# Optimization experiments

Measured on AMD Instinct MI355X. Metric: run time of the kernel, lower is better.

The kernel has to match this reference:

```python
import jax, jax.numpy as jnp
import numpy as np

N = 50000
E = 300000
D_IN = 128
H = 256
D_OUT = 256


def _glorot(key, shape):
    fan_in, fan_out = shape[0], shape[1]
    lim = float(np.sqrt(6.0 / (fan_in + fan_out)))
    return jax.random.uniform(key, shape, jnp.float32, -lim, lim)


def setup_inputs() -> dict:
    key = jax.random.key(0)
    ks = jax.random.split(key, 12)
    x = jax.random.normal(ks[0], (N, D_IN), jnp.float32)
    edge_index = jax.random.randint(ks[1], (2, E), 0, N, jnp.int64)
    return {
        "x": x,
        "edge_index": edge_index,
        "W1": _glorot(ks[2], (D_IN, H)),  "b1": jnp.zeros((H,), jnp.float32),
        "Wg1": _glorot(ks[3], (H, H)),    "bg1": jnp.zeros((H,), jnp.float32),
        "Wg2": _glorot(ks[4], (H, H)),    "bg2": jnp.zeros((H,), jnp.float32),
        "W2": _glorot(ks[5], (H, H)),     "b2": jnp.zeros((H,), jnp.float32),
        "W3": _glorot(ks[6], (H, D_OUT)), "b3": jnp.zeros((D_OUT,), jnp.float32),
    }


def _gcn_conv(h, src, dst, W, b):
    # PyG GCNConv: h' = D^-1/2 (A + I) D^-1/2 (h W) + b, deg counted at target with self-loops
    h = h @ W                                           # [N, H]
    deg = jnp.zeros((N,), h.dtype).at[dst].add(1.0) + 1.0
    dinv = jax.lax.rsqrt(deg)                           # deg^-1/2, [N]
    norm = dinv[src] * dinv[dst]                        # [E]
    msg = h[src] * norm[:, None]                        # gather + scale, [E, H]
    agg = jax.ops.segment_sum(msg, dst, num_segments=N)  # scatter-add
    agg = agg + h * (dinv * dinv)[:, None]              # self-loop contribution (norm = 1/deg)
    return agg + b


def reference(x, edge_index, W1, b1, Wg1, bg1, Wg2, bg2, W2, b2, W3, b3):
    src, dst = edge_index[0], edge_index[1]
    h = jax.nn.relu(x @ W1 + b1)
    h = jax.nn.relu(_gcn_conv(h, src, dst, Wg1, bg1))
    h = jax.nn.relu(_gcn_conv(h, src, dst, Wg2, bg2))
    h = jax.nn.relu(h @ W2 + b2)
    return jax.nn.softmax(h @ W3 + b3, axis=1)
```

## Files before the change

### kernel.cpp

```cpp
#include <hip/hip_runtime.h>
#include <math.h>

#define HDIM 256

typedef float floatx4 __attribute__((ext_vector_type(4)));
typedef __bf16 bf16x8 __attribute__((ext_vector_type(8)));
typedef unsigned short ushortx4 __attribute__((ext_vector_type(4)));
typedef unsigned short ushortx8 __attribute__((ext_vector_type(8)));

#define AS1C(p) ((const __attribute__((address_space(1))) void*)(p))
#define AS3(p)  ((__attribute__((address_space(3))) void*)(p))

__device__ inline unsigned short bf16_rn(float f) {
  unsigned u = __float_as_uint(f);
  return (unsigned short)((u + 0x7FFFu + ((u >> 16) & 1u)) >> 16);
}

__device__ inline void split_f32(float f, unsigned short& h, unsigned short& l) {
  unsigned short hb = bf16_rn(f);
  float hf = __uint_as_float(((unsigned)hb) << 16);
  h = hb;
  l = bf16_rn(f - hf);
}

// ... 92 lines not shown
void scan_final_kernel(const int* __restrict__ deg, const int* __restrict__ boff,
                       int* __restrict__ rowptr, int* __restrict__ cursor, int n) {
  __shared__ int sm[256];
  int t = threadIdx.x;
  int idx = blockIdx.x * 256 + t;
  int v = (idx < n) ? deg[idx] : 0;
  sm[t] = v;
  __syncthreads();
  for (int off = 1; off < 256; off <<= 1) {
    int a = (t >= off) ? sm[t - off] : 0;
    __syncthreads();
    sm[t] += a;
    __syncthreads();
  }
  int excl = sm[t] - v + boff[blockIdx.x];
  if (idx < n) { rowptr[idx] = excl; cursor[idx] = excl; }
}

__global__ __launch_bounds__(256)
void fill_csr_kernel(const int* __restrict__ ei, const float* __restrict__ dinv,
                     int* __restrict__ cursor, int* __restrict__ col,
                     float* __restrict__ wsrc, int E) {
  int e = blockIdx.x * 256 + threadIdx.x;
  if (e < E) {
    int s = ei[e];
    int d = ei[E + e];
    int p = atomicAdd(&cursor[d], 1);
    col[p] = s;
    wsrc[p] = dinv[s];
  }
}


template<bool BIAS, bool RELU>
__global__ __launch_bounds__(512, 4)
void mfma_gemm_sA(const float* __restrict__ A,
                  const unsigned short* __restrict__ SWH, const unsigned short* __restrict__ SWL,
                  const float* __restrict__ bias,
                  unsigned short* __restrict__ CH, unsigned short* __restrict__ CL,
                  int M, int K) {
  __shared__ __align__(16) unsigned short AsH[4096];
  __shared__ __align__(16) unsigned short AsL[4096];
  __shared__ __align__(16) unsigned short BsH[8192];
  __shared__ __align__(16) unsigned short BsL[8192];

  const int tid = threadIdx.x;
  const int w = tid >> 6;
  const int l = tid & 63;
  const int l15 = l & 15;
  const int quad = l >> 4;
  const int wm = w & 1;
  const int wn = w >> 1;
  const int bm = blockIdx.x * 128;
  const int ktc = K >> 5;
  const int chunksPerCb = ktc * 512;

  floatx4 acc[4][4];
#pragma unroll
  for (int i = 0; i < 4; ++i)
#pragma unroll
    for (int j = 0; j < 4; ++j) acc[i][j] = (floatx4){0.f, 0.f, 0.f, 0.f};

  const int arow = tid >> 2;
  const int ap = tid & 3;
  const int akc = ap ^ (arow & 3) ^ ((arow >> 2) & 3);
  int agrow = bm + arow;
  if (agrow > M - 1) agrow = M - 1;
  const float* agp = A + (size_t)agrow * K + akc * 8;

  for (int kt = 0; kt < ktc; ++kt) {
    float4 f0 = *(const float4*)(agp + kt * 32);
    float4 f1 = *(const float4*)(agp + kt * 32 + 4);

    __syncthreads();

#pragma unroll
    for (int j = 0; j < 2; ++j) {
      int pos = j * 512 + w * 64 + l;
      int kc = pos >> 8;
      int within = pos & 255;
      int cb = within >> 7;
      int colL = within & 127;
      size_t gi = (size_t)cb * chunksPerCb + (size_t)kt * 512 + kc * 128 + colL;
      __builtin_amdgcn_global_load_lds(AS1C(SWH + gi * 8),
                                       AS3(&BsH[(j * 512 + w * 64) * 8]), 16, 0, 0);
      __builtin_amdgcn_global_load_lds(AS1C(SWL + gi * 8),
                                       AS3(&BsL[(j * 512 + w * 64) * 8]), 16, 0, 0);
    }

    {
      float f[8] = {f0.x, f0.y, f0.z, f0.w, f1.x, f1.y, f1.z, f1.w};
      ushortx8 hh, ll;
#pragma unroll
      for (int e = 0; e < 8; ++e) {
        unsigned short h, lo;
        split_f32(f[e], h, lo);
        hh[e] = h;
        ll[e] = lo;
      }
      *(ushortx8*)&AsH[(size_t)tid * 8] = hh;
      *(ushortx8*)&AsL[(size_t)tid * 8] = ll;
    }

    __syncthreads();

    bf16x8 aH[4], aL[4];
#pragma unroll
    for (int fi = 0; fi < 4; ++fi) {
      int r = wm * 64 + fi * 16 + l15;
      int sw = quad ^ (r & 3) ^ ((r >> 2) & 3);
      aH[fi] = *(const bf16x8*)&AsH[(r * 4 + sw) * 8];
      aL[fi] = *(const bf16x8*)&AsL[(r * 4 + sw) * 8];
    }
#pragma unroll
    for (int fj = 0; fj < 4; ++fj) {
      int colG = wn * 64 + fj * 16 + l15;
      int cidx = quad * 256 + colG;
      bf16x8 bh = *(const bf16x8*)&BsH[cidx * 8];
      bf16x8 bl = *(const bf16x8*)&BsL[cidx * 8];
#pragma unroll
      for (int fi = 0; fi < 4; ++fi) {
        floatx4 t = acc[fi][fj];
        t = __builtin_amdgcn_mfma_f32_16x16x32_bf16(aH[fi], bl, t, 0, 0, 0);
        t = __builtin_amdgcn_mfma_f32_16x16x32_bf16(aL[fi], bh, t, 0, 0, 0);
        t = __builtin_amdgcn_mfma_f32_16x16x32_bf16(aH[fi], bh, t, 0, 0, 0);
        acc[fi][fj] = t;
      }
    }
  }

  float bcol[4];
#pragma unroll
  for (int fj = 0; fj < 4; ++fj)
    bcol[fj] = BIAS ? bias[wn * 64 + fj * 16 + l15] : 0.f;

#pragma unroll
  for (int fi = 0; fi < 4; ++fi) {
    int rb = bm + wm * 64 + fi * 16 + quad * 4;
#pragma unroll
    for (int r = 0; r < 4; ++r) {
      int row = rb + r;
      if (row < M) {
        size_t base = (size_t)row * HDIM + wn * 64 + l15;
#pragma unroll
        for (int fj = 0; fj < 4; ++fj) {
          float v = acc[fi][fj][r] + bcol[fj];
          if (RELU) v = fmaxf(v, 0.f);
          unsigned short h, lo;
          split_f32(v, h, lo);
          CH[base + fj * 16] = h;
          CL[base + fj * 16] = lo;
        }
      }
    }
  }
}


template<bool BIAS, bool RELU, bool SPLIT_OUT>
__global__ __launch_bounds__(512, 4)
void mfma_gemm_p(const unsigned short* __restrict__ AH, const unsigned short* __restrict__ AL,
                 const unsigned short* __restrict__ SWH, const unsigned short* __restrict__ SWL,
                 const float* __restrict__ bias,
                 float* __restrict__ C, unsigned short* __restrict__ CH,
                 unsigned short* __restrict__ CL, int M, int K) {
  __shared__ __align__(16) unsigned short AsH[4096];
  __shared__ __align__(16) unsigned short AsL[4096];
  __shared__ __align__(16) unsigned short BsH[8192];
  __shared__ __align__(16) unsigned short BsL[8192];

  const int tid = threadIdx.x;
  const int w = tid >> 6;
  const int l = tid & 63;
  const int l15 = l & 15;
  const int quad = l >> 4;
  const int wm = w & 1;
  const int wn = w >> 1;
  const int bm = blockIdx.x * 128;
  const int ktc = K >> 5;
  const int chunksPerCb = ktc * 512;

  floatx4 acc[4][4];
#pragma unroll
  for (int i = 0; i < 4; ++i)
#pragma unroll
    for (int j = 0; j < 4; ++j) acc[i][j] = (floatx4){0.f, 0.f, 0.f, 0.f};

  for (int kt = 0; kt < ktc; ++kt) {
    __syncthreads();

    {
      int L = tid;
      int row = L >> 2;
      int p = L & 3;
      int kc = p ^ (row & 3) ^ ((row >> 2) & 3);
      int grow = bm + row;
      if (grow > M - 1) grow = M - 1;
      const unsigned short* gH = AH + (size_t)grow * K + kt * 32 + kc * 8;
      const unsigned short* gL = AL + (size_t)grow * K + kt * 32 + kc * 8;
      __builtin_amdgcn_global_load_lds(AS1C(gH), AS3(&AsH[(w * 64) * 8]), 16, 0, 0);
      __builtin_amdgcn_global_load_lds(AS1C(gL), AS3(&AsL[(w * 64) * 8]), 16, 0, 0);
    }
#pragma unroll
    for (int j = 0; j < 2; ++j) {
      int pos = j * 512 + w * 64 + l;
      int kc = pos >> 8;
      int within = pos & 255;
      int cb = within >> 7;
      int colL = within & 127;
      size_t gi = (size_t)cb * chunksPerCb + (size_t)kt * 512 + kc * 128 + colL;
      __builtin_amdgcn_global_load_lds(AS1C(SWH + gi * 8),
                                       AS3(&BsH[(j * 512 + w * 64) * 8]), 16, 0, 0);
      __builtin_amdgcn_global_load_lds(AS1C(SWL + gi * 8),
                                       AS3(&BsL[(j * 512 + w * 64) * 8]), 16, 0, 0);
    }

    __syncthreads();

    bf16x8 aH[4], aL[4];
#pragma unroll
    for (int fi = 0; fi < 4; ++fi) {
      int r = wm * 64 + fi * 16 + l15;
      int sw = quad ^ (r & 3) ^ ((r >> 2) & 3);
      aH[fi] = *(const bf16x8*)&AsH[(r * 4 + sw) * 8];
      aL[fi] = *(const bf16x8*)&AsL[(r * 4 + sw) * 8];
    }
#pragma unroll
    for (int fj = 0; fj < 4; ++fj) {
      int colG = wn * 64 + fj * 16 + l15;
      int cidx = quad * 256 + colG;
      bf16x8 bh = *(const bf16x8*)&BsH[cidx * 8];
      bf16x8 bl = *(const bf16x8*)&BsL[cidx * 8];
#pragma unroll
      for (int fi = 0; fi < 4; ++fi) {
        floatx4 t = acc[fi][fj];
        t = __builtin_amdgcn_mfma_f32_16x16x32_bf16(aH[fi], bl, t, 0, 0, 0);
        t = __builtin_amdgcn_mfma_f32_16x16x32_bf16(aL[fi], bh, t, 0, 0, 0);
        t = __builtin_amdgcn_mfma_f32_16x16x32_bf16(aH[fi], bh, t, 0, 0, 0);
        acc[fi][fj] = t;
      }
    }
  }

  float bcol[4];
#pragma unroll
  for (int fj = 0; fj < 4; ++fj)
    bcol[fj] = BIAS ? bias[wn * 64 + fj * 16 + l15] : 0.f;

#pragma unroll
  for (int fi = 0; fi < 4; ++fi) {
    int rb = bm + wm * 64 + fi * 16 + quad * 4;
#pragma unroll
    for (int r = 0; r < 4; ++r) {
      int row = rb + r;
      if (row < M) {
        size_t base = (size_t)row * HDIM + wn * 64 + l15;
        if (SPLIT_OUT) {
#pragma unroll
          for (int fj = 0; fj < 4; ++fj) {
            float v = acc[fi][fj][r] + bcol[fj];
            if (RELU) v = fmaxf(v, 0.f);
            unsigned short h, lo;
            split_f32(v, h, lo);
            CH[base + fj * 16] = h;
            CL[base + fj * 16] = lo;
          }
        } else {
#pragma unroll
          for (int fj = 0; fj < 4; ++fj) {
            float v = acc[fi][fj][r] + bcol[fj];
            if (RELU) v = fmaxf(v, 0.f);
            C[base + fj * 16] = v;
          }
        }
      }
    }
  }
}


__global__ __launch_bounds__(512, 4)
void mfma_gemm_softmax(const unsigned short* __restrict__ AH, const unsigned short* __restrict__ AL,
                       const unsigned short* __restrict__ SWH, const unsigned short* __restrict__ SWL,
                       const float* __restrict__ bias, float* __restrict__ out, int M, int K) {
  __shared__ __align__(16) unsigned short AsH[4096];
  __shared__ __align__(16) unsigned short AsL[4096];
  __shared__ __align__(16) unsigned short BsH[8192];
  __shared__ __align__(16) unsigned short BsL[8192];
  __shared__ float smax[128 * 4];
  __shared__ float ssum[128 * 4];

  const int tid = threadIdx.x;
  const int w = tid >> 6;
  const int l = tid & 63;
  const int l15 = l & 15;
  const int quad = l >> 4;
  const int wm = w & 1;
  const int wn = w >> 1;
  const int bm = blockIdx.x * 128;
  const int ktc = K >> 5;
  const int chunksPerCb = ktc * 512;

  floatx4 acc[4][4];
#pragma unroll
  for (int i = 0; i < 4; ++i)
#pragma unroll
    for (int j = 0; j < 4; ++j) acc[i][j] = (floatx4){0.f, 0.f, 0.f, 0.f};

  for (int kt = 0; kt < ktc; ++kt) {
    __syncthreads();

    {
      int L = tid;
      int row = L >> 2;
      int p = L & 3;
      int kc = p ^ (row & 3) ^ ((row >> 2) & 3);
      int grow = bm + row;
      if (grow > M - 1) grow = M - 1;
      const unsigned short* gH = AH + (size_t)grow * K + kt * 32 + kc * 8;
      const unsigned short* gL = AL + (size_t)grow * K + kt * 32 + kc * 8;
      __builtin_amdgcn_global_load_lds(AS1C(gH), AS3(&AsH[(w * 64) * 8]), 16, 0, 0);
      __builtin_amdgcn_global_load_lds(AS1C(gL), AS3(&AsL[(w * 64) * 8]), 16, 0, 0);
    }
#pragma unroll
    for (int j = 0; j < 2; ++j) {
      int pos = j * 512 + w * 64 + l;
      int kc = pos >> 8;
      int within = pos & 255;
      int cb = within >> 7;
      int colL = within & 127;
      size_t gi = (size_t)cb * chunksPerCb + (size_t)kt * 512 + kc * 128 + colL;
      __builtin_amdgcn_global_load_lds(AS1C(SWH + gi * 8),
                                       AS3(&BsH[(j * 512 + w * 64) * 8]), 16, 0, 0);
      __builtin_amdgcn_global_load_lds(AS1C(SWL + gi * 8),
                                       AS3(&BsL[(j * 512 + w * 64) * 8]), 16, 0, 0);
    }

    __syncthreads();

    bf16x8 aH[4], aL[4];
#pragma unroll
    for (int fi = 0; fi < 4; ++fi) {
      int r = wm * 64 + fi * 16 + l15;
      int sw = quad ^ (r & 3) ^ ((r >> 2) & 3);
      aH[fi] = *(const bf16x8*)&AsH[(r * 4 + sw) * 8];
      aL[fi] = *(const bf16x8*)&AsL[(r * 4 + sw) * 8];
    }
#pragma unroll
    for (int fj = 0; fj < 4; ++fj) {
      int colG = wn * 64 + fj * 16 + l15;
      int cidx = quad * 256 + colG;
      bf16x8 bh = *(const bf16x8*)&BsH[cidx * 8];
      bf16x8 bl = *(const bf16x8*)&BsL[cidx * 8];
#pragma unroll
      for (int fi = 0; fi < 4; ++fi) {
        floatx4 t = acc[fi][fj];
        t = __builtin_amdgcn_mfma_f32_16x16x32_bf16(aH[fi], bl, t, 0, 0, 0);
        t = __builtin_amdgcn_mfma_f32_16x16x32_bf16(aL[fi], bh, t, 0, 0, 0);
        t = __builtin_amdgcn_mfma_f32_16x16x32_bf16(aH[fi], bh, t, 0, 0, 0);
        acc[fi][fj] = t;
      }
    }
  }

  float bcol[4];
#pragma unroll
  for (int fj = 0; fj < 4; ++fj)
    bcol[fj] = bias[wn * 64 + fj * 16 + l15];

#pragma unroll
  for (int fi = 0; fi < 4; ++fi) {
#pragma unroll
    for (int r = 0; r < 4; ++r) {
      float mv = -3.4e38f;
#pragma unroll
      for (int fj = 0; fj < 4; ++fj) mv = fmaxf(mv, acc[fi][fj][r] + bcol[fj]);
#pragma unroll
      for (int off = 1; off < 16; off <<= 1) mv = fmaxf(mv, __shfl_xor(mv, off));
      int row = wm * 64 + fi * 16 + quad * 4 + r;
      if (l15 == 0) smax[row * 4 + wn] = mv;
    }
  }
  __syncthreads();

#pragma unroll
  for (int fi = 0; fi < 4; ++fi) {
#pragma unroll
    for (int r = 0; r < 4; ++r) {
      int row = wm * 64 + fi * 16 + quad * 4 + r;
      float gm = fmaxf(fmaxf(smax[row * 4 + 0], smax[row * 4 + 1]),
                       fmaxf(smax[row * 4 + 2], smax[row * 4 + 3]));
      float s = 0.f;
#pragma unroll
      for (int fj = 0; fj < 4; ++fj) {
        float p = expf(acc[fi][fj][r] + bcol[fj] - gm);
        acc[fi][fj][r] = p;
        s += p;
      }
#pragma unroll
      for (int off = 1; off < 16; off <<= 1) s += __shfl_xor(s, off);
      if (l15 == 0) ssum[row * 4 + wn] = s;
    }
  }
  __syncthreads();

#pragma unroll
  for (int fi = 0; fi < 4; ++fi) {
#pragma unroll
    for (int r = 0; r < 4; ++r) {
      int row = wm * 64 + fi * 16 + quad * 4 + r;
      int grow = bm + row;
      if (grow < M) {
        float inv = 1.0f / (ssum[row * 4 + 0] + ssum[row * 4 + 1] +
                            ssum[row * 4 + 2] + ssum[row * 4 + 3]);
        float* Cp = out + (size_t)grow * HDIM + wn * 64 + l15;
#pragma unroll
        for (int fj = 0; fj < 4; ++fj) Cp[fj * 16] = acc[fi][fj][r] * inv;
      }
    }
  }
}


__global__ __launch_bounds__(256)
void aggregate_b(const float* __restrict__ t, const float* __restrict__ dinv,
                 const int* __restrict__ rowptr, const int* __restrict__ col,
                 const float* __restrict__ wsrc, const float* __restrict__ bias,
                 unsigned short* __restrict__ OH, unsigned short* __restrict__ OL, int n) {
  int gw = (int)((blockIdx.x * 256 + threadIdx.x) >> 6);
  int lane = threadIdx.x & 63;
  if (gw >= n) return;
  float di = dinv[gw];
  float4 v = ((const float4*)(t + (size_t)gw * HDIM))[lane];
  float ss = di * di;
  float a0 = v.x * ss, a1 = v.y * ss, a2 = v.z * ss, a3 = v.w * ss;
  int e0 = rowptr[gw], e1 = rowptr[gw + 1];

  for (int base = e0; base < e1; base += 8) {
    int cs[8];
    float wv[8];
#pragma unroll
    for (int i = 0; i < 8; ++i) {
      int e = base + i;
      if (e > e1 - 1) e = e1 - 1;
      cs[i] = col[e];
      wv[i] = wsrc[e];
    }
    float wg[8];
#pragma unroll
    for (int i = 0; i < 8; ++i)
      wg[i] = (base + i < e1) ? wv[i] * di : 0.f;
    float4 rw[8];
#pragma unroll
    for (int i = 0; i < 8; ++i)
      rw[i] = ((const float4*)(t + (size_t)cs[i] * HDIM))[lane];
#pragma unroll
    for (int i = 0; i < 8; ++i) {
      a0 = fmaf(rw[i].x, wg[i], a0);
      a1 = fmaf(rw[i].y, wg[i], a1);
      a2 = fmaf(rw[i].z, wg[i], a2);
      a3 = fmaf(rw[i].w, wg[i], a3);
    }
  }

// ... 46 lines not shown
  int*   rowptr = (int*)alloc((size_t)(N + 1) * sizeof(int));
  int*   cursor = (int*)alloc((size_t)N * sizeof(int));
  int*   col    = (int*)alloc((size_t)E * sizeof(int));
  float* wcsr   = (float*)alloc((size_t)E * sizeof(float));
  const int nb  = (N + 255) / 256;
  int*   bsum   = (int*)alloc((size_t)nb * sizeof(int));
  int*   boff   = (int*)alloc((size_t)nb * sizeof(int));
  unsigned short* W1sH  = (unsigned short*)alloc((size_t)HDIM * K1 * 2);
  unsigned short* W1sL  = (unsigned short*)alloc((size_t)HDIM * K1 * 2);
  unsigned short* Wg1sH = (unsigned short*)alloc((size_t)HDIM * HDIM * 2);
  unsigned short* Wg1sL = (unsigned short*)alloc((size_t)HDIM * HDIM * 2);
  unsigned short* Wg2sH = (unsigned short*)alloc((size_t)HDIM * HDIM * 2);
  unsigned short* Wg2sL = (unsigned short*)alloc((size_t)HDIM * HDIM * 2);
  unsigned short* W2sH  = (unsigned short*)alloc((size_t)HDIM * HDIM * 2);
  unsigned short* W2sL  = (unsigned short*)alloc((size_t)HDIM * HDIM * 2);
  unsigned short* W3sH  = (unsigned short*)alloc((size_t)HDIM * HDIM * 2);
  unsigned short* W3sL  = (unsigned short*)alloc((size_t)HDIM * HDIM * 2);

  const int ge = (E + 255) / 256;

  const int prepChunks = K1 * 32 + 4 * HDIM * 32;
  prep_w_all<<<(prepChunks + 255) / 256, 256, 0, stream>>>(
      W1, W1sH, W1sL, K1, Wg1, Wg1sH, Wg1sL, Wg2, Wg2sH, Wg2sL,
      W2, W2sH, W2sL, W3, W3sH, W3sL);

  hipMemsetAsync(deg, 0, (size_t)N * sizeof(int), stream);
  deg_count_kernel<<<ge, 256, 0, stream>>>(ei, deg, E);
  block_sum_kernel<<<nb, 256, 0, stream>>>(deg, bsum, dinv, N);
  scan_bsums_kernel<<<1, 256, 0, stream>>>(bsum, boff, rowptr, nb, N);
  scan_final_kernel<<<nb, 256, 0, stream>>>(deg, boff, rowptr, cursor, N);
  fill_csr_kernel<<<ge, 256, 0, stream>>>(ei, dinv, cursor, col, wcsr, E);

  const int g128 = (N + 127) / 128;
  const int gagg = (N + 3) / 4;

  mfma_gemm_sA<true, true><<<g128, 512, 0, stream>>>(x, W1sH, W1sL, b1, PH, PL, N, K1);
  mfma_gemm_p<false, false, false><<<g128, 512, 0, stream>>>(PH, PL, Wg1sH, Wg1sL, nullptr, out, nullptr, nullptr, N, HDIM);
  aggregate_b<<<gagg, 256, 0, stream>>>(out, dinv, rowptr, col, wcsr, bg1, PH, PL, N);
  mfma_gemm_p<false, false, false><<<g128, 512, 0, stream>>>(PH, PL, Wg2sH, Wg2sL, nullptr, out, nullptr, nullptr, N, HDIM);
  aggregate_b<<<gagg, 256, 0, stream>>>(out, dinv, rowptr, col, wcsr, bg2, PH, PL, N);
  mfma_gemm_p<true, true, true><<<g128, 512, 0, stream>>>(PH, PL, W2sH, W2sL, b2, nullptr, PH, PL, N, HDIM);
  mfma_gemm_softmax<<<g128, 512, 0, stream>>>(PH, PL, W3sH, W3sL, b3, out, N, HDIM);
}
```

Before: 383.9 us.

## Double-buffer LDS tiles in the MFMA GEMM kernels to overlap loads with compute

The A and B shared-memory tiles in the three split-bf16 MFMA GEMM kernels are now double-buffered. The loads for the next K-tile are issued before the MFMAs on the current tile run, which removes one barrier per iteration and aims to hide global-to-LDS latency. The cost is twice the LDS per block, roughly 96KB, and the launch-bounds minimum is lowered from 4 to 2 blocks. That likely leaves only one resident 512-thread block per CU, so the kernels lose latency hiding across blocks.

```diff
diff --git a/kernel.cpp b/kernel.cpp
--- a/kernel.cpp
+++ b/kernel.cpp
@@ -149,16 +149,16 @@
 
 
 template<bool BIAS, bool RELU>
-__global__ __launch_bounds__(512, 4)
+__global__ __launch_bounds__(512, 2)
 void mfma_gemm_sA(const float* __restrict__ A,
                   const unsigned short* __restrict__ SWH, const unsigned short* __restrict__ SWL,
                   const float* __restrict__ bias,
                   unsigned short* __restrict__ CH, unsigned short* __restrict__ CL,
                   int M, int K) {
-  __shared__ __align__(16) unsigned short AsH[4096];
-  __shared__ __align__(16) unsigned short AsL[4096];
-  __shared__ __align__(16) unsigned short BsH[8192];
-  __shared__ __align__(16) unsigned short BsL[8192];
+  __shared__ __align__(16) unsigned short AsH[2][4096];
+  __shared__ __align__(16) unsigned short AsL[2][4096];
+  __shared__ __align__(16) unsigned short BsH[2][8192];
+  __shared__ __align__(16) unsigned short BsL[2][8192];
 
   const int tid = threadIdx.x;
   const int w = tid >> 6;
@@ -184,12 +184,7 @@
   if (agrow > M - 1) agrow = M - 1;
   const float* agp = A + (size_t)agrow * K + akc * 8;
 
-  for (int kt = 0; kt < ktc; ++kt) {
-    float4 f0 = *(const float4*)(agp + kt * 32);
-    float4 f1 = *(const float4*)(agp + kt * 32 + 4);
-
-    __syncthreads();
-
+  auto stageB = [&](int kt, int buf) {
 #pragma unroll
     for (int j = 0; j < 2; ++j) {
       int pos = j * 512 + w * 64 + l;
@@ -199,41 +194,58 @@
       int colL = within & 127;
       size_t gi = (size_t)cb * chunksPerCb + (size_t)kt * 512 + kc * 128 + colL;
       __builtin_amdgcn_global_load_lds(AS1C(SWH + gi * 8),
-                                       AS3(&BsH[(j * 512 + w * 64) * 8]), 16, 0, 0);
+                                       AS3(&BsH[buf][(j * 512 + w * 64) * 8]), 16, 0, 0);
       __builtin_amdgcn_global_load_lds(AS1C(SWL + gi * 8),
-                                       AS3(&BsL[(j * 512 + w * 64) * 8]), 16, 0, 0);
-    }
-
-    {
-      float f[8] = {f0.x, f0.y, f0.z, f0.w, f1.x, f1.y, f1.z, f1.w};
-      ushortx8 hh, ll;
-#pragma unroll
-      for (int e = 0; e < 8; ++e) {
-        unsigned short h, lo;
-        split_f32(f[e], h, lo);
-        hh[e] = h;
-        ll[e] = lo;
-      }
-      *(ushortx8*)&AsH[(size_t)tid * 8] = hh;
-      *(ushortx8*)&AsL[(size_t)tid * 8] = ll;
-    }
-
-    __syncthreads();
+                                       AS3(&BsL[buf][(j * 512 + w * 64) * 8]), 16, 0, 0);
+    }
+  };
+
+  auto writeA = [&](float4 f0, float4 f1, int buf) {
+    float f[8] = {f0.x, f0.y, f0.z, f0.w, f1.x, f1.y, f1.z, f1.w};
+    ushortx8 hh, ll;
+#pragma unroll
+    for (int e = 0; e < 8; ++e) {
+      unsigned short h, lo;
+      split_f32(f[e], h, lo);
+      hh[e] = h;
+      ll[e] = lo;
+    }
+    *(ushortx8*)&AsH[buf][(size_t)tid * 8] = hh;
+    *(ushortx8*)&AsL[buf][(size_t)tid * 8] = ll;
+  };
+
+  {
+    float4 f0 = *(const float4*)(agp);
+    float4 f1 = *(const float4*)(agp + 4);
+    stageB(0, 0);
+    writeA(f0, f1, 0);
+  }
+  __syncthreads();
+  int cur = 0;
+
+#pragma unroll 1
+  for (int kt = 0; kt < ktc; ++kt) {
+    if (kt + 1 < ktc) {
+      float4 f0 = *(const float4*)(agp + (kt + 1) * 32);
+      float4 f1 = *(const float4*)(agp + (kt + 1) * 32 + 4);
+      stageB(kt + 1, cur ^ 1);
+      writeA(f0, f1, cur ^ 1);
+    }
 
     bf16x8 aH[4], aL[4];
 #pragma unroll
     for (int fi = 0; fi < 4; ++fi) {
       int r = wm * 64 + fi * 16 + l15;
       int sw = quad ^ (r & 3) ^ ((r >> 2) & 3);
-      aH[fi] = *(const bf16x8*)&AsH[(r * 4 + sw) * 8];
-      aL[fi] = *(const bf16x8*)&AsL[(r * 4 + sw) * 8];
+      aH[fi] = *(const bf16x8*)&AsH[cur][(r * 4 + sw) * 8];
+      aL[fi] = *(const bf16x8*)&AsL[cur][(r * 4 + sw) * 8];
     }
 #pragma unroll
     for (int fj = 0; fj < 4; ++fj) {
       int colG = wn * 64 + fj * 16 + l15;
       int cidx = quad * 256 + colG;
-      bf16x8 bh = *(const bf16x8*)&BsH[cidx * 8];
-      bf16x8 bl = *(const bf16x8*)&BsL[cidx * 8];
+      bf16x8 bh = *(const bf16x8*)&BsH[cur][cidx * 8];
+      bf16x8 bl = *(const bf16x8*)&BsL[cur][cidx * 8];
 #pragma unroll
       for (int fi = 0; fi < 4; ++fi) {
         floatx4 t = acc[fi][fj];
@@ -243,6 +255,9 @@
         acc[fi][fj] = t;
       }
     }
+
+    __syncthreads();
+    cur ^= 1;
   }
 
   float bcol[4];
@@ -274,16 +289,16 @@
 
 
 template<bool BIAS, bool RELU, bool SPLIT_OUT>
-__global__ __launch_bounds__(512, 4)
+__global__ __launch_bounds__(512, 2)
 void mfma_gemm_p(const unsigned short* __restrict__ AH, const unsigned short* __restrict__ AL,
                  const unsigned short* __restrict__ SWH, const unsigned short* __restrict__ SWL,
                  const float* __restrict__ bias,
                  float* __restrict__ C, unsigned short* __restrict__ CH,
                  unsigned short* __restrict__ CL, int M, int K) {
-  __shared__ __align__(16) unsigned short AsH[4096];
-  __shared__ __align__(16) unsigned short AsL[4096];
-  __shared__ __align__(16) unsigned short BsH[8192];
-  __shared__ __align__(16) unsigned short BsL[8192];
+  __shared__ __align__(16) unsigned short AsH[2][4096];
+  __shared__ __align__(16) unsigned short AsL[2][4096];
+  __shared__ __align__(16) unsigned short BsH[2][8192];
+  __shared__ __align__(16) unsigned short BsL[2][8192];
 
   const int tid = threadIdx.x;
   const int w = tid >> 6;
@@ -302,20 +317,17 @@
 #pragma unroll
     for (int j = 0; j < 4; ++j) acc[i][j] = (floatx4){0.f, 0.f, 0.f, 0.f};
 
-  for (int kt = 0; kt < ktc; ++kt) {
-    __syncthreads();
-
+  auto stage = [&](int kt, int buf) {
     {
-      int L = tid;
-      int row = L >> 2;
-      int p = L & 3;
+      int row = tid >> 2;
+      int p = tid & 3;
       int kc = p ^ (row & 3) ^ ((row >> 2) & 3);
       int grow = bm + row;
       if (grow > M - 1) grow = M - 1;
       const unsigned short* gH = AH + (size_t)grow * K + kt * 32 + kc * 8;
       const unsigned short* gL = AL + (size_t)grow * K + kt * 32 + kc * 8;
-      __builtin_amdgcn_global_load_lds(AS1C(gH), AS3(&AsH[(w * 64) * 8]), 16, 0, 0);
-      __builtin_amdgcn_global_load_lds(AS1C(gL), AS3(&AsL[(w * 64) * 8]), 16, 0, 0);
+      __builtin_amdgcn_global_load_lds(AS1C(gH), AS3(&AsH[buf][(w * 64) * 8]), 16, 0, 0);
+      __builtin_amdgcn_global_load_lds(AS1C(gL), AS3(&AsL[buf][(w * 64) * 8]), 16, 0, 0);
     }
 #pragma unroll
     for (int j = 0; j < 2; ++j) {
@@ -326,27 +338,34 @@
       int colL = within & 127;
       size_t gi = (size_t)cb * chunksPerCb + (size_t)kt * 512 + kc * 128 + colL;
       __builtin_amdgcn_global_load_lds(AS1C(SWH + gi * 8),
-                                       AS3(&BsH[(j * 512 + w * 64) * 8]), 16, 0, 0);
+                                       AS3(&BsH[buf][(j * 512 + w * 64) * 8]), 16, 0, 0);
       __builtin_amdgcn_global_load_lds(AS1C(SWL + gi * 8),
-                                       AS3(&BsL[(j * 512 + w * 64) * 8]), 16, 0, 0);
-    }
-
-    __syncthreads();
+                                       AS3(&BsL[buf][(j * 512 + w * 64) * 8]), 16, 0, 0);
+    }
+  };
+
+  stage(0, 0);
+  __syncthreads();
+  int cur = 0;
+
+#pragma unroll 1
+  for (int kt = 0; kt < ktc; ++kt) {
+    if (kt + 1 < ktc) stage(kt + 1, cur ^ 1);
 
     bf16x8 aH[4], aL[4];
 #pragma unroll
     for (int fi = 0; fi < 4; ++fi) {
       int r = wm * 64 + fi * 16 + l15;
       int sw = quad ^ (r & 3) ^ ((r >> 2) & 3);
-      aH[fi] = *(const bf16x8*)&AsH[(r * 4 + sw) * 8];
-      aL[fi] = *(const bf16x8*)&AsL[(r * 4 + sw) * 8];
+      aH[fi] = *(const bf16x8*)&AsH[cur][(r * 4 + sw) * 8];
+      aL[fi] = *(const bf16x8*)&AsL[cur][(r * 4 + sw) * 8];
     }
 #pragma unroll
     for (int fj = 0; fj < 4; ++fj) {
       int colG = wn * 64 + fj * 16 + l15;
       int cidx = quad * 256 + colG;
-      bf16x8 bh = *(const bf16x8*)&BsH[cidx * 8];
-      bf16x8 bl = *(const bf16x8*)&BsL[cidx * 8];
+      bf16x8 bh = *(const bf16x8*)&BsH[cur][cidx * 8];
+      bf16x8 bl = *(const bf16x8*)&BsL[cur][cidx * 8];
 #pragma unroll
       for (int fi = 0; fi < 4; ++fi) {
         floatx4 t = acc[fi][fj];
@@ -356,6 +375,9 @@
         acc[fi][fj] = t;
       }
     }
+
+    __syncthreads();
+    cur ^= 1;
   }
 
   float bcol[4];
@@ -395,14 +417,14 @@
 }
 
 
-__global__ __launch_bounds__(512, 4)
+__global__ __launch_bounds__(512, 2)
 void mfma_gemm_softmax(const unsigned short* __restrict__ AH, const unsigned short* __restrict__ AL,
                        const unsigned short* __restrict__ SWH, const unsigned short* __restrict__ SWL,
                        const float* __restrict__ bias, float* __restrict__ out, int M, int K) {
-  __shared__ __align__(16) unsigned short AsH[4096];
-  __shared__ __align__(16) unsigned short AsL[4096];
-  __shared__ __align__(16) unsigned short BsH[8192];
-  __shared__ __align__(16) unsigned short BsL[8192];
+  __shared__ __align__(16) unsigned short AsH[2][4096];
+  __shared__ __align__(16) unsigned short AsL[2][4096];
+  __shared__ __align__(16) unsigned short BsH[2][8192];
+  __shared__ __align__(16) unsigned short BsL[2][8192];
   __shared__ float smax[128 * 4];
   __shared__ float ssum[128 * 4];
 
@@ -423,20 +445,17 @@
 #pragma unroll
     for (int j = 0; j < 4; ++j) acc[i][j] = (floatx4){0.f, 0.f, 0.f, 0.f};
 
-  for (int kt = 0; kt < ktc; ++kt) {
-    __syncthreads();
-
+  auto stage = [&](int kt, int buf) {
     {
-      int L = tid;
-      int row = L >> 2;
-      int p = L & 3;
+      int row = tid >> 2;
+      int p = tid & 3;
       int kc = p ^ (row & 3) ^ ((row >> 2) & 3);
       int grow = bm + row;
       if (grow > M - 1) grow = M - 1;
       const unsigned short* gH = AH + (size_t)grow * K + kt * 32 + kc * 8;
       const unsigned short* gL = AL + (size_t)grow * K + kt * 32 + kc * 8;
-      __builtin_amdgcn_global_load_lds(AS1C(gH), AS3(&AsH[(w * 64) * 8]), 16, 0, 0);
-      __builtin_amdgcn_global_load_lds(AS1C(gL), AS3(&AsL[(w * 64) * 8]), 16, 0, 0);
+      __builtin_amdgcn_global_load_lds(AS1C(gH), AS3(&AsH[buf][(w * 64) * 8]), 16, 0, 0);
+      __builtin_amdgcn_global_load_lds(AS1C(gL), AS3(&AsL[buf][(w * 64) * 8]), 16, 0, 0);
     }
 #pragma unroll
     for (int j = 0; j < 2; ++j) {
@@ -447,27 +466,34 @@
       int colL = within & 127;
       size_t gi = (size_t)cb * chunksPerCb + (size_t)kt * 512 + kc * 128 + colL;
       __builtin_amdgcn_global_load_lds(AS1C(SWH + gi * 8),
-                                       AS3(&BsH[(j * 512 + w * 64) * 8]), 16, 0, 0);
+                                       AS3(&BsH[buf][(j * 512 + w * 64) * 8]), 16, 0, 0);
       __builtin_amdgcn_global_load_lds(AS1C(SWL + gi * 8),
-                                       AS3(&BsL[(j * 512 + w * 64) * 8]), 16, 0, 0);
-    }
-
-    __syncthreads();
+                                       AS3(&BsL[buf][(j * 512 + w * 64) * 8]), 16, 0, 0);
+    }
+  };
+
+  stage(0, 0);
+  __syncthreads();
+  int cur = 0;
+
+#pragma unroll 1
+  for (int kt = 0; kt < ktc; ++kt) {
+    if (kt + 1 < ktc) stage(kt + 1, cur ^ 1);
 
     bf16x8 aH[4], aL[4];
 #pragma unroll
     for (int fi = 0; fi < 4; ++fi) {
       int r = wm * 64 + fi * 16 + l15;
       int sw = quad ^ (r & 3) ^ ((r >> 2) & 3);
-      aH[fi] = *(const bf16x8*)&AsH[(r * 4 + sw) * 8];
-      aL[fi] = *(const bf16x8*)&AsL[(r * 4 + sw) * 8];
+      aH[fi] = *(const bf16x8*)&AsH[cur][(r * 4 + sw) * 8];
+      aL[fi] = *(const bf16x8*)&AsL[cur][(r * 4 + sw) * 8];
     }
 #pragma unroll
     for (int fj = 0; fj < 4; ++fj) {
       int colG = wn * 64 + fj * 16 + l15;
       int cidx = quad * 256 + colG;
-      bf16x8 bh = *(const bf16x8*)&BsH[cidx * 8];
-      bf16x8 bl = *(const bf16x8*)&BsL[cidx * 8];
+      bf16x8 bh = *(const bf16x8*)&BsH[cur][cidx * 8];
+      bf16x8 bl = *(const bf16x8*)&BsL[cur][cidx * 8];
 #pragma unroll
       for (int fi = 0; fi < 4; ++fi) {
         floatx4 t = acc[fi][fj];
@@ -477,6 +503,9 @@
         acc[fi][fj] = t;
       }
     }
+
+    __syncthreads();
+    cur ^= 1;
   }
 
   float bcol[4];
```

After: 426.3 us. 11.0% more time.

## Fuse back-to-back dense GEMMs and keep the intermediate tile in LDS

Applied to the files above, without the earlier changes.

Adds a two-stage fused GEMM kernel that computes the first product, applies bias and ReLU, and feeds the result straight into the second GEMM through shared memory. It is used for x@W1 followed by @Wg1, and for @W2 followed by @W3 with softmax. This removes the global write and re-read of two full N×256 split-bf16 intermediates and two kernel launches. In exchange the fused kernel holds two accumulator sets, so launch bounds drop to 2 blocks per CU, and only one wave column writes each A tile per k-step while the others wait. The aggregation launches are also split into two half-range launches, which adds launch overhead without an obvious benefit.

```diff
diff --git a/kernel.cpp b/kernel.cpp
--- a/kernel.cpp
+++ b/kernel.cpp
@@ -148,13 +148,283 @@
 }
 
 
-template<bool BIAS, bool RELU>
+template<bool P1F32, bool SOFTMX>
+__global__ __launch_bounds__(512, 2)
+void fused_gemm2(const float* __restrict__ A32,
+                 const unsigned short* __restrict__ APH, const unsigned short* __restrict__ APL,
+                 const unsigned short* __restrict__ SW1H, const unsigned short* __restrict__ SW1L,
+                 const float* __restrict__ bias1,
+                 const unsigned short* __restrict__ SW2H, const unsigned short* __restrict__ SW2L,
+                 const float* __restrict__ bias2,
+                 float* __restrict__ outC, int M, int K1) {
+  __shared__ __align__(16) unsigned short AsH[4096];
+  __shared__ __align__(16) unsigned short AsL[4096];
+  __shared__ __align__(16) unsigned short BsH[8192];
+  __shared__ __align__(16) unsigned short BsL[8192];
+  __shared__ float smax[128 * 4];
+  __shared__ float ssum[128 * 4];
+
+  const int tid = threadIdx.x;
+  const int w = tid >> 6;
+  const int l = tid & 63;
+  const int l15 = l & 15;
+  const int quad = l >> 4;
+  const int wm = w & 1;
+  const int wn = w >> 1;
+  const int bm = blockIdx.x * 128;
+  const int ktc1 = K1 >> 5;
+  const int cPc1 = ktc1 * 512;
+
+  floatx4 acc1[4][4];
+#pragma unroll
+  for (int i = 0; i < 4; ++i)
+#pragma unroll
+    for (int j = 0; j < 4; ++j) acc1[i][j] = (floatx4){0.f, 0.f, 0.f, 0.f};
+
+  const int arow = tid >> 2;
+  const int ap = tid & 3;
+  const int akc = ap ^ (arow & 3) ^ ((arow >> 2) & 3);
+  int agrow = bm + arow;
+  if (agrow > M - 1) agrow = M - 1;
+  const float* agp = P1F32 ? (A32 + (size_t)agrow * K1 + akc * 8) : nullptr;
+
+  for (int kt = 0; kt < ktc1; ++kt) {
+    float4 f0, f1;
+    if (P1F32) {
+      f0 = *(const float4*)(agp + kt * 32);
+      f1 = *(const float4*)(agp + kt * 32 + 4);
+    }
+
+    __syncthreads();
+
+#pragma unroll
+    for (int j = 0; j < 2; ++j) {
+      int pos = j * 512 + w * 64 + l;
+      int kc = pos >> 8;
+      int within = pos & 255;
+      int cb = within >> 7;
+      int colL = within & 127;
+      size_t gi = (size_t)cb * cPc1 + (size_t)kt * 512 + kc * 128 + colL;
+      __builtin_amdgcn_global_load_lds(AS1C(SW1H + gi * 8),
+                                       AS3(&BsH[(j * 512 + w * 64) * 8]), 16, 0, 0);
+      __builtin_amdgcn_global_load_lds(AS1C(SW1L + gi * 8),
+                                       AS3(&BsL[(j * 512 + w * 64) * 8]), 16, 0, 0);
+    }
+
+    if (P1F32) {
+      float f[8] = {f0.x, f0.y, f0.z, f0.w, f1.x, f1.y, f1.z, f1.w};
+      ushortx8 hh, ll;
+#pragma unroll
+      for (int e = 0; e < 8; ++e) {
+        unsigned short h, lo;
+        split_f32(f[e], h, lo);
+        hh[e] = h;
+        ll[e] = lo;
+      }
+      *(ushortx8*)&AsH[(size_t)tid * 8] = hh;
+      *(ushortx8*)&AsL[(size_t)tid * 8] = ll;
+    } else {
+      int row = tid >> 2;
+      int p = tid & 3;
+      int kc = p ^ (row & 3) ^ ((row >> 2) & 3);
+      int grow = bm + row;
+      if (grow > M - 1) grow = M - 1;
+      const unsigned short* gH = APH + (size_t)grow * K1 + kt * 32 + kc * 8;
+      const unsigned short* gL = APL + (size_t)grow * K1 + kt * 32 + kc * 8;
+      __builtin_amdgcn_global_load_lds(AS1C(gH), AS3(&AsH[(w * 64) * 8]), 16, 0, 0);
+      __builtin_amdgcn_global_load_lds(AS1C(gL), AS3(&AsL[(w * 64) * 8]), 16, 0, 0);
+    }
+
+    __syncthreads();
+
+    bf16x8 aH[4], aL[4];
+#pragma unroll
+    for (int fi = 0; fi < 4; ++fi) {
+      int r = wm * 64 + fi * 16 + l15;
+      int sw = quad ^ (r & 3) ^ ((r >> 2) & 3);
+      aH[fi] = *(const bf16x8*)&AsH[(r * 4 + sw) * 8];
+      aL[fi] = *(const bf16x8*)&AsL[(r * 4 + sw) * 8];
+    }
+#pragma unroll
+    for (int fj = 0; fj < 4; ++fj) {
+      int colG = wn * 64 + fj * 16 + l15;
+      int cidx = quad * 256 + colG;
+      bf16x8 bh = *(const bf16x8*)&BsH[cidx * 8];
+      bf16x8 bl = *(const bf16x8*)&BsL[cidx * 8];
+#pragma unroll
+      for (int fi = 0; fi < 4; ++fi) {
+        floatx4 t = acc1[fi][fj];
+        t = __builtin_amdgcn_mfma_f32_16x16x32_bf16(aH[fi], bl, t, 0, 0, 0);
+        t = __builtin_amdgcn_mfma_f32_16x16x32_bf16(aL[fi], bh, t, 0, 0, 0);
+        t = __builtin_amdgcn_mfma_f32_16x16x32_bf16(aH[fi], bh, t, 0, 0, 0);
+        acc1[fi][fj] = t;
+      }
+    }
+  }
+
+  float bcol1[4];
+#pragma unroll
+  for (int fj = 0; fj < 4; ++fj)
+    bcol1[fj] = bias1[wn * 64 + fj * 16 + l15];
+
+  floatx4 acc2[4][4];
+#pragma unroll
+  for (int i = 0; i < 4; ++i)
+#pragma unroll
+    for (int j = 0; j < 4; ++j) acc2[i][j] = (floatx4){0.f, 0.f, 0.f, 0.f};
+
+  const int cPc2 = 8 * 512;
+
+  for (int kt2 = 0; kt2 < 8; ++kt2) {
+    __syncthreads();
+
+    if (wn == (kt2 >> 1)) {
+      int fjb = (kt2 & 1) * 2;
+#pragma unroll
+      for (int fjo = 0; fjo < 2; ++fjo) {
+        int fj = fjb + fjo;
+        int cl = fjo * 16 + l15;
+        int kc = cl >> 3;
+        int e = cl & 7;
+#pragma unroll
+        for (int fi = 0; fi < 4; ++fi) {
+#pragma unroll
+          for (int r = 0; r < 4; ++r) {
+            int R = wm * 64 + fi * 16 + quad * 4 + r;
+            int p = kc ^ (R & 3) ^ ((R >> 2) & 3);
+            float v = fmaxf(acc1[fi][fj][r] + bcol1[fj], 0.f);
+            unsigned short h, lo;
+            split_f32(v, h, lo);
+            AsH[(R * 4 + p) * 8 + e] = h;
+            AsL[(R * 4 + p) * 8 + e] = lo;
+          }
+        }
+      }
+    }
+
+#pragma unroll
+    for (int j = 0; j < 2; ++j) {
+      int pos = j * 512 + w * 64 + l;
+      int kc = pos >> 8;
+      int within = pos & 255;
+      int cb = within >> 7;
+      int colL = within & 127;
+      size_t gi = (size_t)cb * cPc2 + (size_t)kt2 * 512 + kc * 128 + colL;
+      __builtin_amdgcn_global_load_lds(AS1C(SW2H + gi * 8),
+                                       AS3(&BsH[(j * 512 + w * 64) * 8]), 16, 0, 0);
+      __builtin_amdgcn_global_load_lds(AS1C(SW2L + gi * 8),
+                                       AS3(&BsL[(j * 512 + w * 64) * 8]), 16, 0, 0);
+    }
+
+    __syncthreads();
+
+    bf16x8 aH[4], aL[4];
+#pragma unroll
+    for (int fi = 0; fi < 4; ++fi) {
+      int r = wm * 64 + fi * 16 + l15;
+      int sw = quad ^ (r & 3) ^ ((r >> 2) & 3);
+      aH[fi] = *(const bf16x8*)&AsH[(r * 4 + sw) * 8];
+      aL[fi] = *(const bf16x8*)&AsL[(r * 4 + sw) * 8];
+    }
+#pragma unroll
+    for (int fj = 0; fj < 4; ++fj) {
+      int colG = wn * 64 + fj * 16 + l15;
+      int cidx = quad * 256 + colG;
+      bf16x8 bh = *(const bf16x8*)&BsH[cidx * 8];
+      bf16x8 bl = *(const bf16x8*)&BsL[cidx * 8];
+#pragma unroll
+      for (int fi = 0; fi < 4; ++fi) {
+        floatx4 t = acc2[fi][fj];
+        t = __builtin_amdgcn_mfma_f32_16x16x32_bf16(aH[fi], bl, t, 0, 0, 0);
+        t = __builtin_amdgcn_mfma_f32_16x16x32_bf16(aL[fi], bh, t, 0, 0, 0);
+        t = __builtin_amdgcn_mfma_f32_16x16x32_bf16(aH[fi], bh, t, 0, 0, 0);
+        acc2[fi][fj] = t;
+      }
+    }
+  }
+
+  if (SOFTMX) {
+    float bcol2[4];
+#pragma unroll
+    for (int fj = 0; fj < 4; ++fj)
+      bcol2[fj] = bias2[wn * 64 + fj * 16 + l15];
+
+#pragma unroll
+    for (int fi = 0; fi < 4; ++fi) {
+#pragma unroll
+      for (int r = 0; r < 4; ++r) {
+        float mv = -3.4e38f;
+#pragma unroll
+        for (int fj = 0; fj < 4; ++fj) mv = fmaxf(mv, acc2[fi][fj][r] + bcol2[fj]);
+#pragma unroll
+        for (int off = 1; off < 16; off <<= 1) mv = fmaxf(mv, __shfl_xor(mv, off));
+        int row = wm * 64 + fi * 16 + quad * 4 + r;
+        if (l15 == 0) smax[row * 4 + wn] = mv;
+      }
+    }
+    __syncthreads();
+
+#pragma unroll
+    for (int fi = 0; fi < 4; ++fi) {
+#pragma unroll
+      for (int r = 0; r < 4; ++r) {
+        int row = wm * 64 + fi * 16 + quad * 4 + r;
+        float gm = fmaxf(fmaxf(smax[row * 4 + 0], smax[row * 4 + 1]),
+                         fmaxf(smax[row * 4 + 2], smax[row * 4 + 3]));
+        float s = 0.f;
+#pragma unroll
+        for (int fj = 0; fj < 4; ++fj) {
+          float p = expf(acc2[fi][fj][r] + bcol2[fj] - gm);
+          acc2[fi][fj][r] = p;
+          s += p;
+        }
+#pragma unroll
+        for (int off = 1; off < 16; off <<= 1) s += __shfl_xor(s, off);
+        if (l15 == 0) ssum[row * 4 + wn] = s;
+      }
+    }
+    __syncthreads();
+
+#pragma unroll
+    for (int fi = 0; fi < 4; ++fi) {
+#pragma unroll
+      for (int r = 0; r < 4; ++r) {
+        int row = wm * 64 + fi * 16 + quad * 4 + r;
+        int grow = bm + row;
+        if (grow < M) {
+          float inv = 1.0f / (ssum[row * 4 + 0] + ssum[row * 4 + 1] +
+                              ssum[row * 4 + 2] + ssum[row * 4 + 3]);
+          float* Cp = outC + (size_t)grow * HDIM + wn * 64 + l15;
+#pragma unroll
+          for (int fj = 0; fj < 4; ++fj) Cp[fj * 16] = acc2[fi][fj][r] * inv;
+        }
+      }
+    }
+  } else {
+#pragma unroll
+    for (int fi = 0; fi < 4; ++fi) {
+      int rb = bm + wm * 64 + fi * 16 + quad * 4;
+#pragma unroll
+      for (int r = 0; r < 4; ++r) {
+        int row = rb + r;
+        if (row < M) {
+          size_t base = (size_t)row * HDIM + wn * 64 + l15;
+#pragma unroll
+          for (int fj = 0; fj < 4; ++fj) outC[base + fj * 16] = acc2[fi][fj][r];
+        }
+      }
+    }
+  }
+}
+
+
+template<bool BIAS, bool RELU, bool SPLIT_OUT>
 __global__ __launch_bounds__(512, 4)
-void mfma_gemm_sA(const float* __restrict__ A,
-                  const unsigned short* __restrict__ SWH, const unsigned short* __restrict__ SWL,
-                  const float* __restrict__ bias,
-                  unsigned short* __restrict__ CH, unsigned short* __restrict__ CL,
-                  int M, int K) {
+void mfma_gemm_p(const unsigned short* __restrict__ AH, const unsigned short* __restrict__ AL,
+                 const unsigned short* __restrict__ SWH, const unsigned short* __restrict__ SWL,
+                 const float* __restrict__ bias,
+                 float* __restrict__ C, unsigned short* __restrict__ CH,
+                 unsigned short* __restrict__ CL, int M, int K) {
   __shared__ __align__(16) unsigned short AsH[4096];
   __shared__ __align__(16) unsigned short AsL[4096];
   __shared__ __align__(16) unsigned short BsH[8192];
@@ -177,19 +447,21 @@
 #pragma unroll
     for (int j = 0; j < 4; ++j) acc[i][j] = (floatx4){0.f, 0.f, 0.f, 0.f};
 
-  const int arow = tid >> 2;
-  const int ap = tid & 3;
-  const int akc = ap ^ (arow & 3) ^ ((arow >> 2) & 3);
-  int agrow = bm + arow;
-  if (agrow > M - 1) agrow = M - 1;
-  const float* agp = A + (size_t)agrow * K + akc * 8;
-
   for (int kt = 0; kt < ktc; ++kt) {
-    float4 f0 = *(const float4*)(agp + kt * 32);
-    float4 f1 = *(const float4*)(agp + kt * 32 + 4);
-
-    __syncthreads();
-
+    __syncthreads();
+
+    {
+      int L = tid;
+      int row = L >> 2;
+      int p = L & 3;
+      int kc = p ^ (row & 3) ^ ((row >> 2) & 3);
+      int grow = bm + row;
+      if (grow > M - 1) grow = M - 1;
+      const unsigned short* gH = AH + (size_t)grow * K + kt * 32 + kc * 8;
+      const unsigned short* gL = AL + (size_t)grow * K + kt * 32 + kc * 8;
+      __builtin_amdgcn_global_load_lds(AS1C(gH), AS3(&AsH[(w * 64) * 8]), 16, 0, 0);
+      __builtin_amdgcn_global_load_lds(AS1C(gL), AS3(&AsL[(w * 64) * 8]), 16, 0, 0);
+    }
 #pragma unroll
     for (int j = 0; j < 2; ++j) {
       int pos = j * 512 + w * 64 + l;
@@ -204,133 +476,6 @@
                                        AS3(&BsL[(j * 512 + w * 64) * 8]), 16, 0, 0);
     }
 
-    {
-      float f[8] = {f0.x, f0.y, f0.z, f0.w, f1.x, f1.y, f1.z, f1.w};
-      ushortx8 hh, ll;
-#pragma unroll
-      for (int e = 0; e < 8; ++e) {
-        unsigned short h, lo;
-        split_f32(f[e], h, lo);
-        hh[e] = h;
-        ll[e] = lo;
-      }
-      *(ushortx8*)&AsH[(size_t)tid * 8] = hh;
-      *(ushortx8*)&AsL[(size_t)tid * 8] = ll;
-    }
-
-    __syncthreads();
-
-    bf16x8 aH[4], aL[4];
-#pragma unroll
-    for (int fi = 0; fi < 4; ++fi) {
-      int r = wm * 64 + fi * 16 + l15;
-      int sw = quad ^ (r & 3) ^ ((r >> 2) & 3);
-      aH[fi] = *(const bf16x8*)&AsH[(r * 4 + sw) * 8];
-      aL[fi] = *(const bf16x8*)&AsL[(r * 4 + sw) * 8];
-    }
-#pragma unroll
-    for (int fj = 0; fj < 4; ++fj) {
-      int colG = wn * 64 + fj * 16 + l15;
-      int cidx = quad * 256 + colG;
-      bf16x8 bh = *(const bf16x8*)&BsH[cidx * 8];
-      bf16x8 bl = *(const bf16x8*)&BsL[cidx * 8];
-#pragma unroll
-      for (int fi = 0; fi < 4; ++fi) {
-        floatx4 t = acc[fi][fj];
-        t = __builtin_amdgcn_mfma_f32_16x16x32_bf16(aH[fi], bl, t, 0, 0, 0);
-        t = __builtin_amdgcn_mfma_f32_16x16x32_bf16(aL[fi], bh, t, 0, 0, 0);
-        t = __builtin_amdgcn_mfma_f32_16x16x32_bf16(aH[fi], bh, t, 0, 0, 0);
-        acc[fi][fj] = t;
-      }
-    }
-  }
-
-  float bcol[4];
-#pragma unroll
-  for (int fj = 0; fj < 4; ++fj)
-    bcol[fj] = BIAS ? bias[wn * 64 + fj * 16 + l15] : 0.f;
-
-#pragma unroll
-  for (int fi = 0; fi < 4; ++fi) {
-    int rb = bm + wm * 64 + fi * 16 + quad * 4;
-#pragma unroll
-    for (int r = 0; r < 4; ++r) {
-      int row = rb + r;
-      if (row < M) {
-        size_t base = (size_t)row * HDIM + wn * 64 + l15;
-#pragma unroll
-        for (int fj = 0; fj < 4; ++fj) {
-          float v = acc[fi][fj][r] + bcol[fj];
-          if (RELU) v = fmaxf(v, 0.f);
-          unsigned short h, lo;
-          split_f32(v, h, lo);
-          CH[base + fj * 16] = h;
-          CL[base + fj * 16] = lo;
-        }
-      }
-    }
-  }
-}
-
-
-template<bool BIAS, bool RELU, bool SPLIT_OUT>
-__global__ __launch_bounds__(512, 4)
-void mfma_gemm_p(const unsigned short* __restrict__ AH, const unsigned short* __restrict__ AL,
-                 const unsigned short* __restrict__ SWH, const unsigned short* __restrict__ SWL,
-                 const float* __restrict__ bias,
-                 float* __restrict__ C, unsigned short* __restrict__ CH,
-                 unsigned short* __restrict__ CL, int M, int K) {
-  __shared__ __align__(16) unsigned short AsH[4096];
-  __shared__ __align__(16) unsigned short AsL[4096];
-  __shared__ __align__(16) unsigned short BsH[8192];
-  __shared__ __align__(16) unsigned short BsL[8192];
-
-  const int tid = threadIdx.x;
-  const int w = tid >> 6;
-  const int l = tid & 63;
-  const int l15 = l & 15;
-  const int quad = l >> 4;
-  const int wm = w & 1;
-  const int wn = w >> 1;
-  const int bm = blockIdx.x * 128;
-  const int ktc = K >> 5;
-  const int chunksPerCb = ktc * 512;
-
-  floatx4 acc[4][4];
-#pragma unroll
-  for (int i = 0; i < 4; ++i)
-#pragma unroll
-    for (int j = 0; j < 4; ++j) acc[i][j] = (floatx4){0.f, 0.f, 0.f, 0.f};
-
-  for (int kt = 0; kt < ktc; ++kt) {
-    __syncthreads();
-
-    {
-      int L = tid;
-      int row = L >> 2;
-      int p = L & 3;
-      int kc = p ^ (row & 3) ^ ((row >> 2) & 3);
-      int grow = bm + row;
-      if (grow > M - 1) grow = M - 1;
-      const unsigned short* gH = AH + (size_t)grow * K + kt * 32 + kc * 8;
-      const unsigned short* gL = AL + (size_t)grow * K + kt * 32 + kc * 8;
-      __builtin_amdgcn_global_load_lds(AS1C(gH), AS3(&AsH[(w * 64) * 8]), 16, 0, 0);
-      __builtin_amdgcn_global_load_lds(AS1C(gL), AS3(&AsL[(w * 64) * 8]), 16, 0, 0);
-    }
-#pragma unroll
-    for (int j = 0; j < 2; ++j) {
-      int pos = j * 512 + w * 64 + l;
-      int kc = pos >> 8;
-      int within = pos & 255;
-      int cb = within >> 7;
-      int colL = within & 127;
-      size_t gi = (size_t)cb * chunksPerCb + (size_t)kt * 512 + kc * 128 + colL;
-      __builtin_amdgcn_global_load_lds(AS1C(SWH + gi * 8),
-                                       AS3(&BsH[(j * 512 + w * 64) * 8]), 16, 0, 0);
-      __builtin_amdgcn_global_load_lds(AS1C(SWL + gi * 8),
-                                       AS3(&BsL[(j * 512 + w * 64) * 8]), 16, 0, 0);
-    }
-
     __syncthreads();
 
     bf16x8 aH[4], aL[4];
@@ -395,157 +540,15 @@
 }
 
 
-__global__ __launch_bounds__(512, 4)
-void mfma_gemm_softmax(const unsigned short* __restrict__ AH, const unsigned short* __restrict__ AL,
-                       const unsigned short* __restrict__ SWH, const unsigned short* __restrict__ SWL,
-                       const float* __restrict__ bias, float* __restrict__ out, int M, int K) {
-  __shared__ __align__(16) unsigned short AsH[4096];
-  __shared__ __align__(16) unsigned short AsL[4096];
-  __shared__ __align__(16) unsigned short BsH[8192];
-  __shared__ __align__(16) unsigned short BsL[8192];
-  __shared__ float smax[128 * 4];
-  __shared__ float ssum[128 * 4];
-
-  const int tid = threadIdx.x;
-  const int w = tid >> 6;
-  const int l = tid & 63;
-  const int l15 = l & 15;
-  const int quad = l >> 4;
-  const int wm = w & 1;
-  const int wn = w >> 1;
-  const int bm = blockIdx.x * 128;
-  const int ktc = K >> 5;
-  const int chunksPerCb = ktc * 512;
-
-  floatx4 acc[4][4];
-#pragma unroll
-  for (int i = 0; i < 4; ++i)
-#pragma unroll
-    for (int j = 0; j < 4; ++j) acc[i][j] = (floatx4){0.f, 0.f, 0.f, 0.f};
-
-  for (int kt = 0; kt < ktc; ++kt) {
-    __syncthreads();
-
-    {
-      int L = tid;
-      int row = L >> 2;
-      int p = L & 3;
-      int kc = p ^ (row & 3) ^ ((row >> 2) & 3);
-      int grow = bm + row;
-      if (grow > M - 1) grow = M - 1;
-      const unsigned short* gH = AH + (size_t)grow * K + kt * 32 + kc * 8;
-      const unsigned short* gL = AL + (size_t)grow * K + kt * 32 + kc * 8;
-      __builtin_amdgcn_global_load_lds(AS1C(gH), AS3(&AsH[(w * 64) * 8]), 16, 0, 0);
-      __builtin_amdgcn_global_load_lds(AS1C(gL), AS3(&AsL[(w * 64) * 8]), 16, 0, 0);
-    }
-#pragma unroll
-    for (int j = 0; j < 2; ++j) {
-      int pos = j * 512 + w * 64 + l;
-      int kc = pos >> 8;
-      int within = pos & 255;
-      int cb = within >> 7;
-      int colL = within & 127;
-      size_t gi = (size_t)cb * chunksPerCb + (size_t)kt * 512 + kc * 128 + colL;
-      __builtin_amdgcn_global_load_lds(AS1C(SWH + gi * 8),
-                                       AS3(&BsH[(j * 512 + w * 64) * 8]), 16, 0, 0);
-      __builtin_amdgcn_global_load_lds(AS1C(SWL + gi * 8),
-                                       AS3(&BsL[(j * 512 + w * 64) * 8]), 16, 0, 0);
-    }
-
-    __syncthreads();
-
-    bf16x8 aH[4], aL[4];
-#pragma unroll
-    for (int fi = 0; fi < 4; ++fi) {
-      int r = wm * 64 + fi * 16 + l15;
-      int sw = quad ^ (r & 3) ^ ((r >> 2) & 3);
-      aH[fi] = *(const bf16x8*)&AsH[(r * 4 + sw) * 8];
-      aL[fi] = *(const bf16x8*)&AsL[(r * 4 + sw) * 8];
-    }
-#pragma unroll
-    for (int fj = 0; fj < 4; ++fj) {
-      int colG = wn * 64 + fj * 16 + l15;
-      int cidx = quad * 256 + colG;
-      bf16x8 bh = *(const bf16x8*)&BsH[cidx * 8];
-      bf16x8 bl = *(const bf16x8*)&BsL[cidx * 8];
-#pragma unroll
-      for (int fi = 0; fi < 4; ++fi) {
-        floatx4 t = acc[fi][fj];
-        t = __builtin_amdgcn_mfma_f32_16x16x32_bf16(aH[fi], bl, t, 0, 0, 0);
-        t = __builtin_amdgcn_mfma_f32_16x16x32_bf16(aL[fi], bh, t, 0, 0, 0);
-        t = __builtin_amdgcn_mfma_f32_16x16x32_bf16(aH[fi], bh, t, 0, 0, 0);
-        acc[fi][fj] = t;
-      }
-    }
-  }
-
-  float bcol[4];
-#pragma unroll
-  for (int fj = 0; fj < 4; ++fj)
-    bcol[fj] = bias[wn * 64 + fj * 16 + l15];
-
-#pragma unroll
-  for (int fi = 0; fi < 4; ++fi) {
-#pragma unroll
-    for (int r = 0; r < 4; ++r) {
-      float mv = -3.4e38f;
-#pragma unroll
-      for (int fj = 0; fj < 4; ++fj) mv = fmaxf(mv, acc[fi][fj][r] + bcol[fj]);
-#pragma unroll
-      for (int off = 1; off < 16; off <<= 1) mv = fmaxf(mv, __shfl_xor(mv, off));
-      int row = wm * 64 + fi * 16 + quad * 4 + r;
-      if (l15 == 0) smax[row * 4 + wn] = mv;
-    }
-  }
-  __syncthreads();
-
-#pragma unroll
-  for (int fi = 0; fi < 4; ++fi) {
-#pragma unroll
-    for (int r = 0; r < 4; ++r) {
-      int row = wm * 64 + fi * 16 + quad * 4 + r;
-      float gm = fmaxf(fmaxf(smax[row * 4 + 0], smax[row * 4 + 1]),
-                       fmaxf(smax[row * 4 + 2], smax[row * 4 + 3]));
-      float s = 0.f;
-#pragma unroll
-      for (int fj = 0; fj < 4; ++fj) {
-        float p = expf(acc[fi][fj][r] + bcol[fj] - gm);
-        acc[fi][fj][r] = p;
-        s += p;
-      }
-#pragma unroll
-      for (int off = 1; off < 16; off <<= 1) s += __shfl_xor(s, off);
-      if (l15 == 0) ssum[row * 4 + wn] = s;
-    }
-  }
-  __syncthreads();
-
-#pragma unroll
-  for (int fi = 0; fi < 4; ++fi) {
-#pragma unroll
-    for (int r = 0; r < 4; ++r) {
-      int row = wm * 64 + fi * 16 + quad * 4 + r;
-      int grow = bm + row;
-      if (grow < M) {
-        float inv = 1.0f / (ssum[row * 4 + 0] + ssum[row * 4 + 1] +
-                            ssum[row * 4 + 2] + ssum[row * 4 + 3]);
-        float* Cp = out + (size_t)grow * HDIM + wn * 64 + l15;
-#pragma unroll
-        for (int fj = 0; fj < 4; ++fj) Cp[fj * 16] = acc[fi][fj][r] * inv;
-      }
-    }
-  }
-}
-
-
 __global__ __launch_bounds__(256)
 void aggregate_b(const float* __restrict__ t, const float* __restrict__ dinv,
                  const int* __restrict__ rowptr, const int* __restrict__ col,
                  const float* __restrict__ wsrc, const float* __restrict__ bias,
-                 unsigned short* __restrict__ OH, unsigned short* __restrict__ OL, int n) {
-  int gw = (int)((blockIdx.x * 256 + threadIdx.x) >> 6);
+                 unsigned short* __restrict__ OH, unsigned short* __restrict__ OL,
+                 int row0, int nend) {
+  int gw = row0 + (int)((blockIdx.x * 256 + threadIdx.x) >> 6);
   int lane = threadIdx.x & 63;
-  if (gw >= n) return;
+  if (gw >= nend) return;
   float di = dinv[gw];
   float4 v = ((const float4*)(t + (size_t)gw * HDIM))[lane];
   float ss = di * di;
@@ -658,13 +661,17 @@
   fill_csr_kernel<<<ge, 256, 0, stream>>>(ei, dinv, cursor, col, wcsr, E);
 
   const int g128 = (N + 127) / 128;
-  const int gagg = (N + 3) / 4;
-
-  mfma_gemm_sA<true, true><<<g128, 512, 0, stream>>>(x, W1sH, W1sL, b1, PH, PL, N, K1);
-  mfma_gemm_p<false, false, false><<<g128, 512, 0, stream>>>(PH, PL, Wg1sH, Wg1sL, nullptr, out, nullptr, nullptr, N, HDIM);
-  aggregate_b<<<gagg, 256, 0, stream>>>(out, dinv, rowptr, col, wcsr, bg1, PH, PL, N);
+  const int half = (N + 1) / 2;
+  const int gagg1 = (half + 3) / 4;
+  const int gagg2 = (N - half + 3) / 4;
+
+  fused_gemm2<true, false><<<g128, 512, 0, stream>>>(
+      x, nullptr, nullptr, W1sH, W1sL, b1, Wg1sH, Wg1sL, nullptr, out, N, K1);
+  aggregate_b<<<gagg1, 256, 0, stream>>>(out, dinv, rowptr, col, wcsr, bg1, PH, PL, 0, half);
+  aggregate_b<<<gagg2, 256, 0, stream>>>(out, dinv, rowptr, col, wcsr, bg1, PH, PL, half, N);
   mfma_gemm_p<false, false, false><<<g128, 512, 0, stream>>>(PH, PL, Wg2sH, Wg2sL, nullptr, out, nullptr, nullptr, N, HDIM);
-  aggregate_b<<<gagg, 256, 0, stream>>>(out, dinv, rowptr, col, wcsr, bg2, PH, PL, N);
-  mfma_gemm_p<true, true, true><<<g128, 512, 0, stream>>>(PH, PL, W2sH, W2sL, b2, nullptr, PH, PL, N, HDIM);
-  mfma_gemm_softmax<<<g128, 512, 0, stream>>>(PH, PL, W3sH, W3sL, b3, out, N, HDIM);
-}
+  aggregate_b<<<gagg1, 256, 0, stream>>>(out, dinv, rowptr, col, wcsr, bg2, PH, PL, 0, half);
+  aggregate_b<<<gagg2, 256, 0, stream>>>(out, dinv, rowptr, col, wcsr, bg2, PH, PL, half, N);
+  fused_gemm2<false, true><<<g128, 512, 0, stream>>>(
+      nullptr, PH, PL, W2sH, W2sL, b2, W3sH, W3sL, b3, out, N, HDIM);
+}
```

Result: slower. 540.7 us (+40.8%).
